# Optimization experiments

Hardware: AMD Instinct MI355X
Metric: run time of the kernel (lower is better)

The kernel has to match this reference:

```python
import jax, jax.numpy as jnp
import numpy as np

B, T, H = 8192, 24, 1024


def setup_inputs() -> dict:
    key = jax.random.key(0)
    ks = jax.random.split(key, 16)
    n = lambda k, shp, s=1.0: (jax.random.normal(k, shp, dtype=jnp.float32) * s)
    return {
        "x": n(ks[0], (B, T, 1)),
        "h1_0": n(ks[1], (B, H), 0.02),
        "c1_0": n(ks[2], (B, H), 0.02),
        "h2_0": n(ks[3], (B, H), 0.02),
        "c2_0": n(ks[4], (B, H), 0.02),
        "W_ih1": n(ks[5], (4 * H, 1), 0.05),
        "W_hh1": n(ks[6], (4 * H, H), 0.02),
        "b_ih1": n(ks[7], (4 * H,), 0.02),
        "b_hh1": n(ks[8], (4 * H,), 0.02),
        "W_ih2": n(ks[9], (4 * H, H), 0.02),
        "W_hh2": n(ks[10], (4 * H, H), 0.02),
        "b_ih2": n(ks[11], (4 * H,), 0.02),
        "b_hh2": n(ks[12], (4 * H,), 0.02),
        "W_out": n(ks[13], (2, H), 0.02),
        "b_out": jnp.array([0.2, -0.2], dtype=jnp.float32),
    }


def _lstm_cell(x_t, h, c, W_ih, W_hh, b_ih, b_hh):
    # PyTorch LSTMCell: gates ordered (i, f, g, o)
    gates = x_t @ W_ih.T + b_ih + h @ W_hh.T + b_hh  # [B, 4H]
    i, f, g, o = jnp.split(gates, 4, axis=-1)
    c_new = jax.nn.sigmoid(f) * c + jax.nn.sigmoid(i) * jnp.tanh(g)
    h_new = jax.nn.sigmoid(o) * jnp.tanh(c_new)
    return h_new, c_new


def reference(x, h1_0, c1_0, h2_0, c2_0,
              W_ih1, W_hh1, b_ih1, b_hh1,
              W_ih2, W_hh2, b_ih2, b_hh2,
              W_out, b_out):
    xs = jnp.transpose(x, (1, 0, 2))  # [T, B, 1]

    def step(carry, x_t):
        h1, c1, h2, c2 = carry
        h1, c1 = _lstm_cell(x_t, h1, c1, W_ih1, W_hh1, b_ih1, b_hh1)
        h2, c2 = _lstm_cell(h1, h2, c2, W_ih2, W_hh2, b_ih2, b_hh2)
        return (h1, c1, h2, c2), None

    (h1, c1, h2, c2), _ = jax.lax.scan(step, (h1_0, c1_0, h2_0, c2_0), xs)
    return h2 @ W_out.T + b_out  # [B, 2]
```

## Files before the change

### kernel.cpp

```cpp
#include <hip/hip_runtime.h>
#include <hip/hip_bf16.h>
#include <stdint.h>

#define B_SZ 8192
#define T_SZ 24
#define H_SZ 1024
#define G4   4096

typedef __attribute__((ext_vector_type(8))) short bf16x8;
typedef __attribute__((ext_vector_type(4))) float f32x4;

__device__ __forceinline__ int perm_old(int p) {
    int gate = (p >> 4) & 3;
    int unit = ((p >> 6) << 4) | (p & 15);
    return gate * 1024 + unit;
}

__global__ void k_prep_w1(const float* __restrict__ Whh1, __hip_bfloat16* __restrict__ dst) {
    int i = blockIdx.x * blockDim.x + threadIdx.x;
    int p = i >> 10, k = i & 1023;
    dst[i] = __float2bfloat16(Whh1[(size_t)perm_old(p) * 1024 + k]);
}

__global__ void k_prep_w2(const float* __restrict__ Wih2, const float* __restrict__ Whh2,
                          __hip_bfloat16* __restrict__ dst) {
    int i = blockIdx.x * blockDim.x + threadIdx.x;
    int p = i >> 11, k = i & 2047;
    int old = perm_old(p);
    float v = (k < 1024) ? Wih2[(size_t)old * 1024 + k] : Whh2[(size_t)old * 1024 + (k - 1024)];
    dst[i] = __float2bfloat16(v);
}

__global__ void k_prep_vec(const float* __restrict__ bih1, const float* __restrict__ bhh1,
                           const float* __restrict__ bih2, const float* __restrict__ bhh2,
                           const float* __restrict__ Wih1,
                           float* __restrict__ b1p, float* __restrict__ b2p,
                           float* __restrict__ w1p) {
    int p = blockIdx.x * blockDim.x + threadIdx.x;
    if (p >= G4) return;
    int old = perm_old(p);
    b1p[p] = bih1[old] + bhh1[old];
    b2p[p] = bih2[old] + bhh2[old];
    w1p[p] = Wih1[old];
}

__global__ void k_xT(const float* __restrict__ x, float* __restrict__ xT) {
    int i = blockIdx.x * blockDim.x + threadIdx.x;
    if (i >= B_SZ * T_SZ) return;
    int b = i / T_SZ, t = i % T_SZ;
    xT[t * B_SZ + b] = x[i];
}

__global__ void k_init_state(const float* __restrict__ h1_0, const float* __restrict__ c1_0,
                             const float* __restrict__ h2_0, const float* __restrict__ c2_0,
                             __hip_bfloat16* __restrict__ A2_0, __hip_bfloat16* __restrict__ A2_1,
                             float* __restrict__ c1, float* __restrict__ c2) {
    int i = blockIdx.x * blockDim.x + threadIdx.x;
    if (i >= B_SZ * H_SZ) return;
    int b = i >> 10, j = i & 1023;
    A2_1[(size_t)b * 2048 + j]        = __float2bfloat16(h1_0[i]);
    A2_0[(size_t)b * 2048 + 1024 + j] = __float2bfloat16(h2_0[i]);
    c1[i] = c1_0[i];
    c2[i] = c2_0[i];
}

#define BM 256
#define BN 256
#define BK 64

template<int LAYER>
__global__ __launch_bounds__(512, 2)
void k_gemm_cell(const __hip_bfloat16* __restrict__ A, int lda,
                 const __hip_bfloat16* __restrict__ Bw, int ldb, int K,
                 const float* __restrict__ biasp, const float* __restrict__ wih1p,
                 const float* __restrict__ xT, int t,
                 float* __restrict__ c, __hip_bfloat16* __restrict__ hout) {
    __shared__ short As[2][BM][BK];
    __shared__ short Bs[2][BN][BK];
    const int tid  = threadIdx.x;
    const int lane = tid & 63;
    const int wid  = tid >> 6;

    const int bid = blockIdx.x;
    const int swz = (bid & 7) * 64 + (bid >> 3);
    const int n0 = (swz & 15) * BN;
    const int m0 = (swz >> 4) * BM;

    const int wm = wid >> 2;
    const int wn = wid & 3;
    const int fr = lane & 15;
    const int kg = lane >> 4;

    f32x4 acc[8][4];
#pragma unroll
    for (int i = 0; i < 8; ++i)
#pragma unroll
        for (int j = 0; j < 4; ++j) acc[i][j] = (f32x4)0.f;

    auto stage = [&](int kt, int buf) {
#pragma unroll
        for (int it = 0; it < 4; ++it) {
            int cbase = it * 512 + wid * 64;
            int ci  = cbase + lane;
            int row = ci >> 3, cr = ci & 7;
            int scol = ((cr ^ (row & 7)) << 3);
            const __hip_bfloat16* ga = A  + (size_t)(m0 + row) * lda + kt * BK + scol;
            const __hip_bfloat16* gb = Bw + (size_t)(n0 + row) * ldb + kt * BK + scol;
            __builtin_amdgcn_global_load_lds(
                (const __attribute__((address_space(1))) void*)ga,
                (__attribute__((address_space(3))) void*)(&As[buf][0][0] + (size_t)cbase * 8),
                16, 0, 0);
            __builtin_amdgcn_global_load_lds(
                (const __attribute__((address_space(1))) void*)gb,
                (__attribute__((address_space(3))) void*)(&Bs[buf][0][0] + (size_t)cbase * 8),
                16, 0, 0);
        }
    };

    const int NK = K >> 6;
    stage(0, 0);
    stage(1, 1);

    for (int kt = 0; kt < NK; ++kt) {
        const int buf = kt & 1;
        if (kt + 1 < NK) asm volatile("s_waitcnt vmcnt(8)" ::: "memory");
        else             asm volatile("s_waitcnt vmcnt(0)" ::: "memory");
        __builtin_amdgcn_s_barrier();
        asm volatile("" ::: "memory");

        __builtin_amdgcn_s_setprio(1);
#pragma unroll
        for (int ks = 0; ks < 2; ++ks) {
            bf16x8 bfrag[4];
#pragma unroll
            for (int n = 0; n < 4; ++n) {
                int row = wn * 64 + n * 16 + fr;
                int chunk = (ks * 4 + kg) ^ (row & 7);
                bfrag[n] = *(const bf16x8*)&Bs[buf][row][chunk * 8];
            }
#pragma unroll
            for (int m = 0; m < 8; ++m) {
                int row = wm * 128 + m * 16 + fr;
                int chunk = (ks * 4 + kg) ^ (row & 7);
                bf16x8 afrag = *(const bf16x8*)&As[buf][row][chunk * 8];
#pragma unroll
                for (int n = 0; n < 4; ++n)
                    acc[m][n] = __builtin_amdgcn_mfma_f32_16x16x32_bf16(afrag, bfrag[n], acc[m][n], 0, 0, 0);
            }
        }
        __builtin_amdgcn_s_setprio(0);

        asm volatile("" ::: "memory");
        __builtin_amdgcn_s_barrier();
        asm volatile("" ::: "memory");
        if (kt + 2 < NK) stage(kt + 2, buf);
    }

    float biasv[4], xwv[4];
#pragma unroll
    for (int n = 0; n < 4; ++n) {
        int col = n0 + wn * 64 + n * 16 + fr;
        biasv[n] = biasp[col];
        if (LAYER == 1) xwv[n] = wih1p[col];
    }
    const int u = ((n0 >> 6) + wn) * 16 + fr;

#pragma unroll
    for (int m = 0; m < 8; ++m) {
        int rbase = m0 + wm * 128 + m * 16 + (lane >> 4) * 4;
#pragma unroll
        for (int j = 0; j < 4; ++j) {
            int b = rbase + j;
            float gi = acc[m][0][j] + biasv[0];
            float gf = acc[m][1][j] + biasv[1];
            float gg = acc[m][2][j] + biasv[2];
            float go = acc[m][3][j] + biasv[3];
            if (LAYER == 1) {
                float xv = xT[t * B_SZ + b];
                gi += xv * xwv[0];
                gf += xv * xwv[1];
                gg += xv * xwv[2];
                go += xv * xwv[3];
            }
            float si = 1.f / (1.f + __expf(-gi));
            float sf = 1.f / (1.f + __expf(-gf));
            float so = 1.f / (1.f + __expf(-go));
            float tg = tanhf(gg);
            size_t ci = (size_t)b * H_SZ + u;
            float cn = sf * c[ci] + si * tg;
            c[ci] = cn;
            hout[(size_t)b * 2048 + u] = __float2bfloat16(so * tanhf(cn));
        }
    }
}

__global__ __launch_bounds__(256)
void k_out(const __hip_bfloat16* __restrict__ h2base, const float* __restrict__ Wout,
           const float* __restrict__ bout, float* __restrict__ out) {
    int gw   = (blockIdx.x * blockDim.x + threadIdx.x) >> 6;
    int lane = threadIdx.x & 63;
    if (gw >= B_SZ) return;
    const __hip_bfloat16* h = h2base + (size_t)gw * 2048;
    float a0 = 0.f, a1 = 0.f;
#pragma unroll
    for (int k = lane; k < 1024; k += 64) {
        float hv = __bfloat162float(h[k]);
        a0 += hv * Wout[k];
        a1 += hv * Wout[1024 + k];
    }
    for (int off = 32; off; off >>= 1) {
        a0 += __shfl_down(a0, off);
        a1 += __shfl_down(a1, off);
    }
    if (lane == 0) {
        out[gw * 2 + 0] = a0 + bout[0];
        out[gw * 2 + 1] = a1 + bout[1];
    }
}

extern "C" void kernel_launch(void* const* d_in, const int* in_sizes, int n_in,
                              void* d_out, int out_size, void* d_ws, size_t ws_size,
                              hipStream_t stream) {
    const float* x    = (const float*)d_in[0];
    const float* h1_0 = (const float*)d_in[1];
    const float* c1_0 = (const float*)d_in[2];
    const float* h2_0 = (const float*)d_in[3];
    const float* c2_0 = (const float*)d_in[4];
    const float* Wih1 = (const float*)d_in[5];
    const float* Whh1 = (const float*)d_in[6];
    const float* bih1 = (const float*)d_in[7];
    const float* bhh1 = (const float*)d_in[8];
    const float* Wih2 = (const float*)d_in[9];
    const float* Whh2 = (const float*)d_in[10];
    const float* bih2 = (const float*)d_in[11];
    const float* bhh2 = (const float*)d_in[12];
    const float* Wout = (const float*)d_in[13];
    const float* bout = (const float*)d_in[14];
    float* out = (float*)d_out;
    (void)in_sizes; (void)n_in; (void)out_size; (void)ws_size;

    uint8_t* ws = (uint8_t*)d_ws;
    size_t off = 0;
    auto alloc = [&](size_t bytes) { void* p = ws + off; off += (bytes + 255) & ~(size_t)255; return p; };
    __hip_bfloat16* A2_0  = (__hip_bfloat16*)alloc((size_t)B_SZ * 2048 * 2);
    __hip_bfloat16* A2_1  = (__hip_bfloat16*)alloc((size_t)B_SZ * 2048 * 2);
    float*          c1    = (float*)alloc((size_t)B_SZ * H_SZ * 4);
    float*          c2    = (float*)alloc((size_t)B_SZ * H_SZ * 4);
    __hip_bfloat16* Whh1p = (__hip_bfloat16*)alloc((size_t)G4 * H_SZ * 2);
    __hip_bfloat16* Wcat2p= (__hip_bfloat16*)alloc((size_t)G4 * 2048 * 2);
    float*          bias1p= (float*)alloc(G4 * 4);
    float*          bias2p= (float*)alloc(G4 * 4);
    float*          wih1p = (float*)alloc(G4 * 4);
    float*          xT    = (float*)alloc((size_t)T_SZ * B_SZ * 4);

    __hip_bfloat16* A2[2] = { A2_0, A2_1 };

    k_prep_w1<<<(G4 * H_SZ + 255) / 256, 256, 0, stream>>>(Whh1, Whh1p);
    k_prep_w2<<<(G4 * 2048 + 255) / 256, 256, 0, stream>>>(Wih2, Whh2, Wcat2p);
    k_prep_vec<<<(G4 + 255) / 256, 256, 0, stream>>>(bih1, bhh1, bih2, bhh2, Wih1,
                                                     bias1p, bias2p, wih1p);
    k_xT<<<(B_SZ * T_SZ + 255) / 256, 256, 0, stream>>>(x, xT);
    k_init_state<<<(B_SZ * H_SZ + 255) / 256, 256, 0, stream>>>(h1_0, c1_0, h2_0, c2_0,
                                                                A2_0, A2_1, c1, c2);

    const int gemm_blocks = (B_SZ / BM) * (G4 / BN);

    for (int t = 0; t < T_SZ; ++t) {
        __hip_bfloat16* Pprev = A2[(t + 1) & 1];
        __hip_bfloat16* Pt    = A2[t & 1];
        k_gemm_cell<1><<<gemm_blocks, 512, 0, stream>>>(
            (const __hip_bfloat16*)Pprev, 2048, Whh1p, 1024, 1024,
            bias1p, wih1p, xT, t, c1, Pt);
        k_gemm_cell<2><<<gemm_blocks, 512, 0, stream>>>(
            (const __hip_bfloat16*)Pt, 2048, Wcat2p, 2048, 2048,
            bias2p, nullptr, nullptr, 0, c2, A2[(t + 1) & 1] + 1024);
    }
    k_out<<<(B_SZ * 64 + 255) / 256, 256, 0, stream>>>(A2_0 + 1024, Wout, bout, out);
}
```

Measured before the change: 5.885 ms.

## Split GEMM k-tile into four quadrant phases interleaving LDS staging with MFMA

Restructures the main GEMM loop into four sub-phases, each covering one quadrant of the warp's output tile. Each phase reads A/B fragments into registers, issues a slice of the next tile's global-to-LDS loads, then runs its MFMAs. Loads are spread across phases with explicit vmcnt/lgkmcnt waits and sched barriers, so memory traffic overlaps compute instead of arriving in one burst per k-tile. The cost is many more barriers per iteration and intricate wait-count bookkeeping, where a wrong count could cause a race.

```diff
diff --git a/kernel.cpp b/kernel.cpp
--- a/kernel.cpp
+++ b/kernel.cpp
@@ -91,69 +91,172 @@
     const int fr = lane & 15;
     const int kg = lane >> 4;
 
+    const __hip_bfloat16* Abase = A  + (size_t)m0 * lda;
+    const __hip_bfloat16* Bbase = Bw + (size_t)n0 * ldb;
+
     f32x4 acc[8][4];
 #pragma unroll
     for (int i = 0; i < 8; ++i)
 #pragma unroll
         for (int j = 0; j < 4; ++j) acc[i][j] = (f32x4)0.f;
 
-    auto stage = [&](int kt, int buf) {
-#pragma unroll
-        for (int it = 0; it < 4; ++it) {
-            int cbase = it * 512 + wid * 64;
-            int ci  = cbase + lane;
-            int row = ci >> 3, cr = ci & 7;
-            int scol = ((cr ^ (row & 7)) << 3);
-            const __hip_bfloat16* ga = A  + (size_t)(m0 + row) * lda + kt * BK + scol;
-            const __hip_bfloat16* gb = Bw + (size_t)(n0 + row) * ldb + kt * BK + scol;
-            __builtin_amdgcn_global_load_lds(
-                (const __attribute__((address_space(1))) void*)ga,
-                (__attribute__((address_space(3))) void*)(&As[buf][0][0] + (size_t)cbase * 8),
-                16, 0, 0);
-            __builtin_amdgcn_global_load_lds(
-                (const __attribute__((address_space(1))) void*)gb,
-                (__attribute__((address_space(3))) void*)(&Bs[buf][0][0] + (size_t)cbase * 8),
-                16, 0, 0);
-        }
+    auto stage8A = [&](int buf, int lr0, int kcol) {
+        int lr = lr0 + (lane >> 3);
+        int cr = lane & 7;
+        int scol = ((cr ^ (lr & 7)) << 3);
+        const __hip_bfloat16* gp = Abase + (size_t)lr * lda + kcol + scol;
+        __builtin_amdgcn_global_load_lds(
+            (const __attribute__((address_space(1))) void*)gp,
+            (__attribute__((address_space(3))) void*)(&As[buf][lr0][0]), 16, 0, 0);
+    };
+    auto stage8B = [&](int buf, int lr0, int kcol) {
+        int lr = lr0 + (lane >> 3);
+        int cr = lane & 7;
+        int scol = ((cr ^ (lr & 7)) << 3);
+        const __hip_bfloat16* gp = Bbase + (size_t)lr * ldb + kcol + scol;
+        __builtin_amdgcn_global_load_lds(
+            (const __attribute__((address_space(1))) void*)gp,
+            (__attribute__((address_space(3))) void*)(&Bs[buf][lr0][0]), 16, 0, 0);
+    };
+    auto stage_u1 = [&](int kt, int buf) {
+#pragma unroll
+        for (int j = 0; j < 2; ++j) {
+            int rr0 = (wid * 2 + j) * 8;
+            int lr0 = (rr0 < 64) ? rr0 : rr0 + 64;
+            stage8A(buf, lr0, kt * BK);
+        }
+    };
+    auto stage_u2 = [&](int kt, int buf) {
+#pragma unroll
+        for (int j = 0; j < 2; ++j) {
+            int rr0 = (wid * 2 + j) * 8;
+            int lr0 = (rr0 < 64) ? rr0 + 64 : rr0 + 128;
+            stage8A(buf, lr0, kt * BK);
+        }
+    };
+    auto stage_u3 = [&](int kt, int buf) {
+#pragma unroll
+        for (int j = 0; j < 2; ++j) {
+            int rr0 = (wid * 2 + j) * 8;
+            int lr0 = ((rr0 >> 5) << 6) + (rr0 & 31);
+            stage8B(buf, lr0, kt * BK);
+        }
+    };
+    auto stage_u4 = [&](int kt, int buf) {
+#pragma unroll
+        for (int j = 0; j < 2; ++j) {
+            int rr0 = (wid * 2 + j) * 8;
+            int lr0 = ((rr0 >> 5) << 6) + 32 + (rr0 & 31);
+            stage8B(buf, lr0, kt * BK);
+        }
+    };
+
+    auto rdA = [&](int buf, int m, int ks) -> bf16x8 {
+        int row = wm * 128 + m * 16 + fr;
+        int chunk = (ks * 4 + kg) ^ (row & 7);
+        return *(const bf16x8*)&As[buf][row][chunk * 8];
+    };
+    auto rdB = [&](int buf, int n, int ks) -> bf16x8 {
+        int row = wn * 64 + n * 16 + fr;
+        int chunk = (ks * 4 + kg) ^ (row & 7);
+        return *(const bf16x8*)&Bs[buf][row][chunk * 8];
     };
 
     const int NK = K >> 6;
-    stage(0, 0);
-    stage(1, 1);
+
+    stage_u1(0, 0); stage_u3(0, 0); stage_u2(0, 0); stage_u4(0, 0);
+    stage_u1(1, 1); stage_u3(1, 1);
+    asm volatile("s_waitcnt vmcnt(8)" ::: "memory");
+    __builtin_amdgcn_s_barrier();
+
+    bf16x8 a0[4][2], a1[4][2], b0[2][2], b1[2][2];
 
     for (int kt = 0; kt < NK; ++kt) {
         const int buf = kt & 1;
-        if (kt + 1 < NK) asm volatile("s_waitcnt vmcnt(8)" ::: "memory");
+
+#pragma unroll
+        for (int m = 0; m < 4; ++m)
+#pragma unroll
+            for (int ks = 0; ks < 2; ++ks) a0[m][ks] = rdA(buf, m, ks);
+#pragma unroll
+        for (int n = 0; n < 2; ++n)
+#pragma unroll
+            for (int ks = 0; ks < 2; ++ks) b0[n][ks] = rdB(buf, n, ks);
+        if (kt + 1 < NK) stage_u2(kt + 1, buf ^ 1);
+        asm volatile("" ::: "memory");
+        __builtin_amdgcn_s_barrier();
+        asm volatile("s_waitcnt lgkmcnt(0)" ::: "memory");
+        __builtin_amdgcn_sched_barrier(0);
+        __builtin_amdgcn_s_setprio(1);
+#pragma unroll
+        for (int ks = 0; ks < 2; ++ks)
+#pragma unroll
+            for (int m = 0; m < 4; ++m)
+#pragma unroll
+                for (int n = 0; n < 2; ++n)
+                    acc[m][n] = __builtin_amdgcn_mfma_f32_16x16x32_bf16(a0[m][ks], b0[n][ks], acc[m][n], 0, 0, 0);
+        __builtin_amdgcn_s_setprio(0);
+        if (kt + 1 < NK) asm volatile("s_waitcnt vmcnt(6)" ::: "memory");
         else             asm volatile("s_waitcnt vmcnt(0)" ::: "memory");
         __builtin_amdgcn_s_barrier();
-        asm volatile("" ::: "memory");
-
+
+#pragma unroll
+        for (int n = 0; n < 2; ++n)
+#pragma unroll
+            for (int ks = 0; ks < 2; ++ks) b1[n][ks] = rdB(buf, 2 + n, ks);
+        if (kt + 1 < NK) stage_u4(kt + 1, buf ^ 1);
+        asm volatile("" ::: "memory");
+        __builtin_amdgcn_s_barrier();
+        asm volatile("s_waitcnt lgkmcnt(0)" ::: "memory");
+        __builtin_amdgcn_sched_barrier(0);
         __builtin_amdgcn_s_setprio(1);
 #pragma unroll
-        for (int ks = 0; ks < 2; ++ks) {
-            bf16x8 bfrag[4];
-#pragma unroll
-            for (int n = 0; n < 4; ++n) {
-                int row = wn * 64 + n * 16 + fr;
-                int chunk = (ks * 4 + kg) ^ (row & 7);
-                bfrag[n] = *(const bf16x8*)&Bs[buf][row][chunk * 8];
-            }
-#pragma unroll
-            for (int m = 0; m < 8; ++m) {
-                int row = wm * 128 + m * 16 + fr;
-                int chunk = (ks * 4 + kg) ^ (row & 7);
-                bf16x8 afrag = *(const bf16x8*)&As[buf][row][chunk * 8];
-#pragma unroll
-                for (int n = 0; n < 4; ++n)
-                    acc[m][n] = __builtin_amdgcn_mfma_f32_16x16x32_bf16(afrag, bfrag[n], acc[m][n], 0, 0, 0);
-            }
-        }
+        for (int ks = 0; ks < 2; ++ks)
+#pragma unroll
+            for (int m = 0; m < 4; ++m)
+#pragma unroll
+                for (int n = 0; n < 2; ++n)
+                    acc[m][2 + n] = __builtin_amdgcn_mfma_f32_16x16x32_bf16(a0[m][ks], b1[n][ks], acc[m][2 + n], 0, 0, 0);
         __builtin_amdgcn_s_setprio(0);
-
-        asm volatile("" ::: "memory");
-        __builtin_amdgcn_s_barrier();
-        asm volatile("" ::: "memory");
-        if (kt + 2 < NK) stage(kt + 2, buf);
+        asm volatile("" ::: "memory");
+        __builtin_amdgcn_s_barrier();
+
+#pragma unroll
+        for (int m = 0; m < 4; ++m)
+#pragma unroll
+            for (int ks = 0; ks < 2; ++ks) a1[m][ks] = rdA(buf, 4 + m, ks);
+        if (kt + 2 < NK) stage_u1(kt + 2, buf);
+        asm volatile("" ::: "memory");
+        __builtin_amdgcn_s_barrier();
+        asm volatile("s_waitcnt lgkmcnt(0)" ::: "memory");
+        __builtin_amdgcn_sched_barrier(0);
+        __builtin_amdgcn_s_setprio(1);
+#pragma unroll
+        for (int ks = 0; ks < 2; ++ks)
+#pragma unroll
+            for (int m = 0; m < 4; ++m)
+#pragma unroll
+                for (int n = 0; n < 2; ++n)
+                    acc[4 + m][n] = __builtin_amdgcn_mfma_f32_16x16x32_bf16(a1[m][ks], b0[n][ks], acc[4 + m][n], 0, 0, 0);
+        __builtin_amdgcn_s_setprio(0);
+        asm volatile("" ::: "memory");
+        __builtin_amdgcn_s_barrier();
+
+        if (kt + 2 < NK) stage_u3(kt + 2, buf);
+        asm volatile("" ::: "memory");
+        __builtin_amdgcn_s_barrier();
+        __builtin_amdgcn_s_setprio(1);
+#pragma unroll
+        for (int ks = 0; ks < 2; ++ks)
+#pragma unroll
+            for (int m = 0; m < 4; ++m)
+#pragma unroll
+                for (int n = 0; n < 2; ++n)
+                    acc[4 + m][2 + n] = __builtin_amdgcn_mfma_f32_16x16x32_bf16(a1[m][ks], b1[n][ks], acc[4 + m][2 + n], 0, 0, 0);
+        __builtin_amdgcn_s_setprio(0);
+        if (kt + 2 < NK)      asm volatile("s_waitcnt vmcnt(8)" ::: "memory");
+        else if (kt + 1 < NK) asm volatile("s_waitcnt vmcnt(4)" ::: "memory");
+        __builtin_amdgcn_s_barrier();
     }
 
     float biasv[4], xwv[4];
```

Result: faster. 5.535 ms (-5.9%).
